# Kernel optimization log

Measured on AMD Instinct MI355X. Metric: run time of the kernel, lower is better.

Reference implementation:

```python
import jax, jax.numpy as jnp
import numpy as np

N_NODES = 100000
N_EDGES = 1600000
IN_DIM = 64
HEADS = [4, 4]
DIMS = [16, 16]


def gat_layer(x, src, dst, W, al, ar, b, n_nodes):
    """DGL-style GATConv: x [N,F] -> [N,H,D]."""
    H, D = al.shape
    z = (x @ W).reshape(-1, H, D)                      # [N,H,D]
    el = jnp.sum(z * al, axis=-1)                      # [N,H]
    er = jnp.sum(z * ar, axis=-1)                      # [N,H]
    e = jax.nn.leaky_relu(el[src] + er[dst], 0.2)      # [E,H] edge scores
    # numerically-stable edge softmax over incoming edges of each dst node
    m = jax.ops.segment_max(e, dst, num_segments=n_nodes)
    m = jnp.where(jnp.isfinite(m), m, 0.0)
    ex = jnp.exp(e - jax.lax.stop_gradient(m)[dst])    # [E,H]
    denom = jax.ops.segment_sum(ex, dst, num_segments=n_nodes)
    alpha = ex / jnp.maximum(denom[dst], 1e-9)         # [E,H]
    # scatter-aggregate messages alpha * z[src]
    out = jax.ops.segment_sum(alpha[:, :, None] * z[src], dst, num_segments=n_nodes)
    return out + b.reshape(H, D)


def setup_inputs() -> dict:
    key = jax.random.key(0)
    ks = jax.random.split(key, 16)
    feat = jax.random.normal(ks[0], (N_NODES, IN_DIM), dtype=jnp.float32)
    src = jax.random.randint(ks[1], (N_EDGES,), 0, N_NODES, dtype=jnp.int32)
    dst = jax.random.randint(ks[2], (N_EDGES,), 0, N_NODES, dtype=jnp.int32)
    def lin(k, fi, fo):
        return jax.random.normal(k, (fi, fo), dtype=jnp.float32) * (1.0 / np.sqrt(fi))
    H0, D0 = HEADS[0], DIMS[0]
    H1, D1 = HEADS[1], DIMS[1]
    inp = {
        "feat": feat, "src": src, "dst": dst,
        "W0": lin(ks[3], IN_DIM, H0 * D0),
        "al0": jax.random.normal(ks[4], (H0, D0), jnp.float32) * 0.1,
        "ar0": jax.random.normal(ks[5], (H0, D0), jnp.float32) * 0.1,
        "b0": jnp.zeros((H0 * D0,), jnp.float32),
        "W1": lin(ks[6], H0 * D0, H1 * D1),
        "al1": jax.random.normal(ks[7], (H1, D1), jnp.float32) * 0.1,
        "ar1": jax.random.normal(ks[8], (H1, D1), jnp.float32) * 0.1,
        "b1": jnp.zeros((H1 * D1,), jnp.float32),
        "Wo": lin(ks[9], H1 * D1, 1),
        "alo": jax.random.normal(ks[10], (1, 1), jnp.float32) * 0.1,
        "aro": jax.random.normal(ks[11], (1, 1), jnp.float32) * 0.1,
        "bo": jnp.zeros((1,), jnp.float32),
    }
    return inp


def reference(feat, src, dst, W0, al0, ar0, b0, W1, al1, ar1, b1, Wo, alo, aro, bo):
    n = feat.shape[0]
    h = gat_layer(feat, src, dst, W0, al0, ar0, b0, n)       # [N,H0,D0]
    h = jax.nn.relu(h).reshape(n, -1)                         # head concat
    h = gat_layer(h, src, dst, W1, al1, ar1, b1, n)           # [N,H1,D1]
    h = jax.nn.relu(h).reshape(n, -1)
    out = gat_layer(h, src, dst, Wo, alo, aro, bo, n)         # [N,1,1]
    return jnp.squeeze(out, axis=1)                           # [N,1]
```

## Files before the change

kernel.cpp:

```cpp
#include <hip/hip_runtime.h>
#include <hip/hip_fp16.h>
#include <math.h>

#define NN 100000
#define NE 1600000
#define NBUK 391
#define CAP 4608
#define EPB 4096

__device__ __forceinline__ float leaky02(float v) {
    return v > 0.0f ? v : 0.2f * v;
}


__global__ __launch_bounds__(256) void k_bucket(
    const int* __restrict__ src, const int* __restrict__ dst,
    int* __restrict__ bucketCnt, int* __restrict__ gBuf)
{
    __shared__ int stg[EPB];
    __shared__ int tgt[EPB];
    __shared__ int lcnt[NBUK];
    __shared__ int lexc[NBUK];
    __shared__ int lgb[NBUK];
    __shared__ int totalLocal;
    const int t = threadIdx.x;
    const int e0 = blockIdx.x * EPB;

    for (int i = t; i < NBUK; i += 256) lcnt[i] = 0;
    __syncthreads();

    int bk[16], pk[16];
    #pragma unroll
    for (int j = 0; j < 16; ++j) {
        const int e = e0 + j * 256 + t;
        if (e < NE) {
            const int d = dst[e];
            bk[j] = d >> 8;
            pk[j] = (src[e] << 8) | (d & 255);
            atomicAdd(&lcnt[bk[j]], 1);
        } else bk[j] = -1;
    }
    __syncthreads();

    if (t < 64) {
        int carry = 0;
        for (int c = 0; c < NBUK; c += 64) {
            const int idx = c + t;
            int v = (idx < NBUK) ? lcnt[idx] : 0;
            int inc = v;
            #pragma unroll
            for (int off = 1; off < 64; off <<= 1) {
                int u = __shfl_up(inc, off, 64);
                if (t >= off) inc += u;
            }
            if (idx < NBUK) lexc[idx] = carry + inc - v;
            carry += __shfl(inc, 63, 64);
        }
        if (t == 0) totalLocal = carry;
    }
    __syncthreads();

    for (int i = t; i < NBUK; i += 256) {
        const int c = lcnt[i];
        lgb[i] = c ? atomicAdd(&bucketCnt[i], c) : 0;
        lcnt[i] = 0;
    }
    __syncthreads();

    #pragma unroll
    for (int j = 0; j < 16; ++j) {
        if (bk[j] >= 0) {
            const int r = atomicAdd(&lcnt[bk[j]], 1);
            const int p = lexc[bk[j]] + r;
            stg[p] = pk[j];
            int slot = lgb[bk[j]] + r;
            if (slot >= CAP) slot = CAP - 1;
            tgt[p] = bk[j] * CAP + slot;
        }
    }
    __syncthreads();

    const int tot = totalLocal;
    for (int i = t; i < tot; i += 256)
        gBuf[tgt[i]] = stg[i];
}

__global__ __launch_bounds__(256) void k_csr_local(
    const int* __restrict__ bucketCnt, const int* __restrict__ gBuf,
    int* __restrict__ row_ptr, int* __restrict__ ssrc)
{
    __shared__ int stg2[CAP];
    __shared__ int stg3[CAP];
    __shared__ int c2[256];
    __shared__ int sc[256];
    __shared__ int red[256];
    const int t = threadIdx.x;
    const int k = blockIdx.x;
    const int cnt = min(bucketCnt[k], CAP);

    int part = 0;
    for (int j = t; j < k; j += 256) part += bucketCnt[j];
    red[t] = part;
    __syncthreads();
    for (int s2 = 128; s2; s2 >>= 1) {
        if (t < s2) red[t] += red[t + s2];
        __syncthreads();
    }
    const int gb = red[0];

    c2[t] = 0;
    __syncthreads();
    for (int i = t; i < cnt; i += 256) {
        const int pk = gBuf[k * CAP + i];
        stg2[i] = pk;
        atomicAdd(&c2[pk & 255], 1);
    }
    __syncthreads();
    if (t < 64) {
        int carry = 0;
        for (int c = 0; c < 256; c += 64) {
            int v = c2[c + t];
            int inc = v;
            #pragma unroll
            for (int off = 1; off < 64; off <<= 1) {
                int u = __shfl_up(inc, off, 64);
                if (t >= off) inc += u;
            }
            sc[c + t] = carry + inc - v;
            carry += __shfl(inc, 63, 64);
        }
    }
    __syncthreads();
    const int node = (k << 8) + t;
    if (node < NN) row_ptr[node] = gb + sc[t];
    if (k == NBUK - 1 && t == 0) row_ptr[NN] = NE;
    c2[t] = 0;
    __syncthreads();
    for (int i = t; i < cnt; i += 256) {
        const int pk = stg2[i];
        const int dl = pk & 255;
        const int r = atomicAdd(&c2[dl], 1);
        stg3[sc[dl] + r] = pk >> 8;
    }
    __syncthreads();
    for (int i = t; i < cnt; i += 256)
        ssrc[gb + i] = stg3[i];
}


__global__ __launch_bounds__(256) void k_node_prep(
    const float* __restrict__ xin, const float* __restrict__ W,
    const float* __restrict__ al, const float* __restrict__ ar,
    __half* __restrict__ z, float* __restrict__ el, float* __restrict__ er)
{
    const int t = threadIdx.x;
    const int lane = t & 63;
    const int wvU = __builtin_amdgcn_readfirstlane(t >> 6);
    const int nodeBase = blockIdx.x * 64 + wvU * 16;

    float wc[64];
    #pragma unroll
    for (int k = 0; k < 64; ++k) wc[k] = W[k * 64 + lane];
    const float a_l = al[lane], a_r = ar[lane];

    #pragma unroll 1
    for (int i = 0; i < 16; i += 2) {
        const int nA = nodeBase + i;
        if (nA >= NN) break;
        const int nB = nA + 1;
        const bool hasB = (nB < NN);
        const float4* __restrict__ xA4 = (const float4*)(xin + (size_t)nA * 64);
        const float4* __restrict__ xB4 = (const float4*)(xin + (size_t)(hasB ? nB : nA) * 64);

        float accA = 0.f, accB = 0.f;
        #pragma unroll
        for (int k4 = 0; k4 < 16; ++k4) {
            const float4 a4 = xA4[k4];
            const float4 b4 = xB4[k4];
            const float w0 = wc[k4 * 4 + 0], w1 = wc[k4 * 4 + 1];
            const float w2 = wc[k4 * 4 + 2], w3 = wc[k4 * 4 + 3];
            accA += a4.x * w0 + a4.y * w1 + a4.z * w2 + a4.w * w3;
            accB += b4.x * w0 + b4.y * w1 + b4.z * w2 + b4.w * w3;
        }

        {
            z[(size_t)nA * 64 + lane] = __float2half(accA);
            float pl = accA * a_l, pr = accA * a_r;
            #pragma unroll
            for (int off = 8; off > 0; off >>= 1) {
                pl += __shfl_xor(pl, off, 16);
                pr += __shfl_xor(pr, off, 16);
            }
            if ((lane & 15) == 0) {
                const int h = lane >> 4;
                el[nA * 4 + h] = pl;
                er[nA * 4 + h] = pr;
            }
        }
        if (hasB) {
            z[(size_t)nB * 64 + lane] = __float2half(accB);
            float pl = accB * a_l, pr = accB * a_r;
            #pragma unroll
            for (int off = 8; off > 0; off >>= 1) {
                pl += __shfl_xor(pl, off, 16);
                pr += __shfl_xor(pr, off, 16);
            }
            if ((lane & 15) == 0) {
                const int h = lane >> 4;
                el[nB * 4 + h] = pl;
                er[nB * 4 + h] = pr;
            }
        }
    }
}

__global__ __launch_bounds__(256) void k_csr_agg(
    const int* __restrict__ row_ptr, const int* __restrict__ ssrc,
    const float* __restrict__ el, const float* __restrict__ er,
    const __half* __restrict__ z, const float* __restrict__ b,
    float* __restrict__ xout,
    const float* __restrict__ Wo,
    float* __restrict__ zo)
{
    const int t = threadIdx.x;
    const int wv = t >> 6, l = t & 63;
    const int sg = l >> 4, sl = l & 15, hh = sl >> 2;
    const int n = blockIdx.x * 4 + wv;
    const int beg = row_ptr[n], end = row_ptr[n + 1];
    const float er_hh = er[n * 4 + hh];

    float4 acc = {0.f, 0.f, 0.f, 0.f};
    float den = 0.f;
    int i = beg + sg;
    for (; i + 12 < end; i += 16) {
        const int s0 = ssrc[i], s1 = ssrc[i + 4];
        const int s2 = ssrc[i + 8], s3 = ssrc[i + 12];
        const float x0 = __expf(leaky02(el[s0 * 4 + hh] + er_hh));
        const float x1 = __expf(leaky02(el[s1 * 4 + hh] + er_hh));
        const float x2 = __expf(leaky02(el[s2 * 4 + hh] + er_hh));
        const float x3 = __expf(leaky02(el[s3 * 4 + hh] + er_hh));
        const uint2 r0 = *(const uint2*)(z + (size_t)s0 * 64 + sl * 4);
        const uint2 r1 = *(const uint2*)(z + (size_t)s1 * 64 + sl * 4);
        const uint2 r2 = *(const uint2*)(z + (size_t)s2 * 64 + sl * 4);
        const uint2 r3 = *(const uint2*)(z + (size_t)s3 * 64 + sl * 4);
        den += (x0 + x1) + (x2 + x3);
        float2 p;
        p = __half22float2(*(const __half2*)&r0.x); acc.x += x0 * p.x; acc.y += x0 * p.y;
        p = __half22float2(*(const __half2*)&r0.y); acc.z += x0 * p.x; acc.w += x0 * p.y;
        p = __half22float2(*(const __half2*)&r1.x); acc.x += x1 * p.x; acc.y += x1 * p.y;
        p = __half22float2(*(const __half2*)&r1.y); acc.z += x1 * p.x; acc.w += x1 * p.y;
        p = __half22float2(*(const __half2*)&r2.x); acc.x += x2 * p.x; acc.y += x2 * p.y;
        p = __half22float2(*(const __half2*)&r2.y); acc.z += x2 * p.x; acc.w += x2 * p.y;
        p = __half22float2(*(const __half2*)&r3.x); acc.x += x3 * p.x; acc.y += x3 * p.y;
        p = __half22float2(*(const __half2*)&r3.y); acc.z += x3 * p.x; acc.w += x3 * p.y;
    }
    for (; i < end; i += 4) {
        const int s0 = ssrc[i];
        const float x0 = __expf(leaky02(el[s0 * 4 + hh] + er_hh));
        const uint2 r0 = *(const uint2*)(z + (size_t)s0 * 64 + sl * 4);
        den += x0;
        float2 p;
        p = __half22float2(*(const __half2*)&r0.x); acc.x += x0 * p.x; acc.y += x0 * p.y;
        p = __half22float2(*(const __half2*)&r0.y); acc.z += x0 * p.x; acc.w += x0 * p.y;
    }

    #pragma unroll
    for (int off = 16; off < 64; off <<= 1) {
        acc.x += __shfl_xor(acc.x, off, 64);
        acc.y += __shfl_xor(acc.y, off, 64);
        acc.z += __shfl_xor(acc.z, off, 64);
        acc.w += __shfl_xor(acc.w, off, 64);
        den   += __shfl_xor(den,   off, 64);
    }
    const float dinv = 1.0f / fmaxf(den, 1e-9f);

    const float4 b4 = *(const float4*)(b + sl * 4);
    float4 v;
    v.x = fmaxf(acc.x * dinv + b4.x, 0.f);
    v.y = fmaxf(acc.y * dinv + b4.y, 0.f);
    v.z = fmaxf(acc.z * dinv + b4.z, 0.f);
    v.w = fmaxf(acc.w * dinv + b4.w, 0.f);

    if (xout) {
        if (l < 16) *(float4*)(xout + (size_t)n * 64 + sl * 4) = v;
    } else {
        const float4 w4 = *(const float4*)(Wo + sl * 4);
        float p = v.x * w4.x + v.y * w4.y + v.z * w4.z + v.w * w4.w;
        #pragma unroll
        for (int off = 1; off < 16; off <<= 1) p += __shfl_xor(p, off, 64);
        if (l == 0) zo[n] = p;
    }
}


__global__ __launch_bounds__(256) void k_csr_agg_o(
    const int* __restrict__ row_ptr, const int* __restrict__ ssrc,
    const float* __restrict__ zo, const float* __restrict__ alo,
    const float* __restrict__ aro, const float* __restrict__ bo,
    float* __restrict__ out)
{
    const int t = threadIdx.x, l = t & 15;
    const int n = blockIdx.x * 16 + (t >> 4);
    const float a = alo[0];
    const float zr = aro[0] * zo[n];
    const int beg = row_ptr[n], end = row_ptr[n + 1];

    float den = 0.f, accv = 0.f;
    for (int i = beg + l; i < end; i += 16) {
        const float zs = zo[ssrc[i]];
        const float ex = __expf(leaky02(a * zs + zr));
        den += ex; accv += ex * zs;
    }
    #pragma unroll
    for (int off = 8; off; off >>= 1) {
        den  += __shfl_xor(den, off, 16);
        accv += __shfl_xor(accv, off, 16);
    }
    if (l == 0) out[n] = accv / fmaxf(den, 1e-9f) + bo[0];
}


extern "C" void kernel_launch(void* const* d_in, const int* in_sizes, int n_in,
                              void* d_out, int out_size, void* d_ws, size_t ws_size,
                              hipStream_t stream) {
    const float* feat = (const float*)d_in[0];
    const int*   src  = (const int*)d_in[1];
    const int*   dst  = (const int*)d_in[2];
    const float* W0   = (const float*)d_in[3];
    const float* al0  = (const float*)d_in[4];
    const float* ar0  = (const float*)d_in[5];
    const float* b0   = (const float*)d_in[6];
    const float* W1   = (const float*)d_in[7];
    const float* al1  = (const float*)d_in[8];
    const float* ar1  = (const float*)d_in[9];
    const float* b1   = (const float*)d_in[10];
    const float* Wo   = (const float*)d_in[11];
    const float* alo  = (const float*)d_in[12];
    const float* aro  = (const float*)d_in[13];
    const float* bo   = (const float*)d_in[14];
    float* out = (float*)d_out;

    int* bucketCnt  = (int*)d_ws;
    int* row_ptr    = bucketCnt + NBUK;
    int* gBuf       = row_ptr + (NN + 2);
    int* ssrc       = gBuf + (size_t)NBUK * CAP;
    uintptr_t pa = ((uintptr_t)(ssrc + NE) + 15) & ~(uintptr_t)15;
    __half* z  = (__half*)pa;
    float* xA  = (float*)(z + (size_t)NN * 64);
    float* el  = xA + (size_t)NN * 64;
    float* er  = el + (size_t)NN * 4;
    float* zo  = er + (size_t)NN * 4;

    const int gBkt  = (NE + EPB - 1) / EPB;
    const int gPrep = (NN + 63) / 64;
    const int gN16  = NN / 16;
    const int gAgg  = NN / 4;

    hipMemsetAsync(bucketCnt, 0, NBUK * sizeof(int), stream);
    k_bucket   <<<gBkt, 256, 0, stream>>>(src, dst, bucketCnt, gBuf);
    k_csr_local<<<NBUK, 256, 0, stream>>>(bucketCnt, gBuf, row_ptr, ssrc);

    k_node_prep<<<gPrep, 256, 0, stream>>>(feat, W0, al0, ar0, z, el, er);
    k_csr_agg  <<<gAgg, 256, 0, stream>>>(row_ptr, ssrc, el, er, z, b0,
                                          xA, nullptr, nullptr);

    k_node_prep<<<gPrep, 256, 0, stream>>>(xA, W1, al1, ar1, z, el, er);
    k_csr_agg  <<<gAgg, 256, 0, stream>>>(row_ptr, ssrc, el, er, z, b1,
                                          nullptr, Wo, zo);

    k_csr_agg_o<<<gN16, 256, 0, stream>>>(row_ptr, ssrc, zo, alo, aro, bo, out);
}
```

Before: 275.6 us.

## Fuse CSR build with layer-0 prep and split aggregation into two source-range passes

Bucketing and CSR construction now run in the same launches as the layer-0 node transform, so independent blocks overlap and two kernel boundaries disappear. The CSR also sorts each destination's edges by whether the source index falls in the lower or upper half of nodes. Aggregation then runs in two passes, one per source half, with partial sums stored in accT/denT. The aim is to shrink the gathered z working set per pass so it stays cache-resident, at the cost of extra launches and extra global traffic for the partial accumulators.

```diff
diff --git a/kernel.cpp b/kernel.cpp
--- a/kernel.cpp
+++ b/kernel.cpp
@@ -7,13 +7,17 @@
 #define NBUK 391
 #define CAP 4608
 #define EPB 4096
+#define FATA_PREP 782
+#define PREP_BLKS 1563
+#define SPLIT 50000
 
 __device__ __forceinline__ float leaky02(float v) {
     return v > 0.0f ? v : 0.2f * v;
 }
 
 
-__global__ __launch_bounds__(256) void k_bucket(
+__device__ __forceinline__ void bucket_body(
+    const int bid, const int t,
     const int* __restrict__ src, const int* __restrict__ dst,
     int* __restrict__ bucketCnt, int* __restrict__ gBuf)
 {
@@ -23,8 +27,7 @@
     __shared__ int lexc[NBUK];
     __shared__ int lgb[NBUK];
     __shared__ int totalLocal;
-    const int t = threadIdx.x;
-    const int e0 = blockIdx.x * EPB;
+    const int e0 = bid * EPB;
 
     for (int i = t; i < NBUK; i += 256) lcnt[i] = 0;
     __syncthreads();
@@ -85,17 +88,16 @@
         gBuf[tgt[i]] = stg[i];
 }
 
-__global__ __launch_bounds__(256) void k_csr_local(
+__device__ __forceinline__ void csr_body(
+    const int k, const int t,
     const int* __restrict__ bucketCnt, const int* __restrict__ gBuf,
-    int* __restrict__ row_ptr, int* __restrict__ ssrc)
+    int* __restrict__ row_ptr2, int* __restrict__ ssrc)
 {
     __shared__ int stg2[CAP];
     __shared__ int stg3[CAP];
-    __shared__ int c2[256];
-    __shared__ int sc[256];
+    __shared__ int c9[512];
+    __shared__ int sc9[512];
     __shared__ int red[256];
-    const int t = threadIdx.x;
-    const int k = blockIdx.x;
     const int cnt = min(bucketCnt[k], CAP);
 
     int part = 0;
@@ -108,55 +110,59 @@
     }
     const int gb = red[0];
 
-    c2[t] = 0;
+    c9[t] = 0; c9[t + 256] = 0;
     __syncthreads();
     for (int i = t; i < cnt; i += 256) {
         const int pk = gBuf[k * CAP + i];
         stg2[i] = pk;
-        atomicAdd(&c2[pk & 255], 1);
+        const int key = ((pk & 255) << 1) | ((pk >> 8) >= SPLIT ? 1 : 0);
+        atomicAdd(&c9[key], 1);
     }
     __syncthreads();
     if (t < 64) {
         int carry = 0;
-        for (int c = 0; c < 256; c += 64) {
-            int v = c2[c + t];
+        for (int c = 0; c < 512; c += 64) {
+            int v = c9[c + t];
             int inc = v;
             #pragma unroll
             for (int off = 1; off < 64; off <<= 1) {
                 int u = __shfl_up(inc, off, 64);
                 if (t >= off) inc += u;
             }
-            sc[c + t] = carry + inc - v;
+            sc9[c + t] = carry + inc - v;
             carry += __shfl(inc, 63, 64);
         }
     }
     __syncthreads();
-    const int node = (k << 8) + t;
-    if (node < NN) row_ptr[node] = gb + sc[t];
-    if (k == NBUK - 1 && t == 0) row_ptr[NN] = NE;
-    c2[t] = 0;
+    #pragma unroll
+    for (int j = 0; j < 2; ++j) {
+        const int i = t + 256 * j;
+        const int node = (k << 8) + (i >> 1);
+        if (node < NN) row_ptr2[node * 2 + (i & 1)] = gb + sc9[i];
+    }
+    if (k == NBUK - 1 && t == 0) row_ptr2[2 * NN] = NE;
+    c9[t] = 0; c9[t + 256] = 0;
     __syncthreads();
     for (int i = t; i < cnt; i += 256) {
         const int pk = stg2[i];
-        const int dl = pk & 255;
-        const int r = atomicAdd(&c2[dl], 1);
-        stg3[sc[dl] + r] = pk >> 8;
+        const int key = ((pk & 255) << 1) | ((pk >> 8) >= SPLIT ? 1 : 0);
+        const int r = atomicAdd(&c9[key], 1);
+        stg3[sc9[key] + r] = pk >> 8;
     }
     __syncthreads();
     for (int i = t; i < cnt; i += 256)
         ssrc[gb + i] = stg3[i];
 }
 
-
-__global__ __launch_bounds__(256) void k_node_prep(
+__device__ __forceinline__ void prep_body(
+    const int pb, const int t,
     const float* __restrict__ xin, const float* __restrict__ W,
     const float* __restrict__ al, const float* __restrict__ ar,
     __half* __restrict__ z, float* __restrict__ el, float* __restrict__ er)
 {
-    const int t = threadIdx.x;
     const int lane = t & 63;
     const int wvU = __builtin_amdgcn_readfirstlane(t >> 6);
-    const int nodeBase = blockIdx.x * 64 + wvU * 16;
+    const int nodeBase = pb * 64 + wvU * 16;
 
     float wc[64];
     #pragma unroll
@@ -214,10 +220,49 @@
     }
 }
 
-__global__ __launch_bounds__(256) void k_csr_agg(
-    const int* __restrict__ row_ptr, const int* __restrict__ ssrc,
+
+__global__ __launch_bounds__(256) void k_fatA(
+    const int* __restrict__ src, const int* __restrict__ dst,
+    int* __restrict__ bucketCnt, int* __restrict__ gBuf,
+    const float* __restrict__ feat, const float* __restrict__ W0,
+    const float* __restrict__ al0, const float* __restrict__ ar0,
+    __half* __restrict__ z, float* __restrict__ el, float* __restrict__ er)
+{
+    const int t = threadIdx.x;
+    if (blockIdx.x < NBUK)
+        bucket_body(blockIdx.x, t, src, dst, bucketCnt, gBuf);
+    else
+        prep_body(blockIdx.x - NBUK, t, feat, W0, al0, ar0, z, el, er);
+}
+
+__global__ __launch_bounds__(256) void k_fatB(
+    const int* __restrict__ bucketCnt, const int* __restrict__ gBuf,
+    int* __restrict__ row_ptr2, int* __restrict__ ssrc,
+    const float* __restrict__ feat, const float* __restrict__ W0,
+    const float* __restrict__ al0, const float* __restrict__ ar0,
+    __half* __restrict__ z, float* __restrict__ el, float* __restrict__ er)
+{
+    const int t = threadIdx.x;
+    if (blockIdx.x < NBUK)
+        csr_body(blockIdx.x, t, bucketCnt, gBuf, row_ptr2, ssrc);
+    else
+        prep_body(FATA_PREP + (blockIdx.x - NBUK), t, feat, W0, al0, ar0, z, el, er);
+}
+
+__global__ __launch_bounds__(256) void k_node_prep(
+    const float* __restrict__ xin, const float* __restrict__ W,
+    const float* __restrict__ al, const float* __restrict__ ar,
+    __half* __restrict__ z, float* __restrict__ el, float* __restrict__ er)
+{
+    prep_body(blockIdx.x, threadIdx.x, xin, W, al, ar, z, el, er);
+}
+
+__global__ __launch_bounds__(256) void k_agg_pass(
+    const int* __restrict__ row_ptr2, const int* __restrict__ ssrc,
     const float* __restrict__ el, const float* __restrict__ er,
     const __half* __restrict__ z, const float* __restrict__ b,
+    float* __restrict__ accT, float* __restrict__ denT,
+    const int pass,
     float* __restrict__ xout,
     const float* __restrict__ Wo,
     float* __restrict__ zo)
@@ -226,8 +271,16 @@
     const int wv = t >> 6, l = t & 63;
     const int sg = l >> 4, sl = l & 15, hh = sl >> 2;
     const int n = blockIdx.x * 4 + wv;
-    const int beg = row_ptr[n], end = row_ptr[n + 1];
+    const int beg = row_ptr2[2 * n + pass];
+    const int end = row_ptr2[2 * n + pass + 1];
     const float er_hh = er[n * 4 + hh];
+
+    float4 prev = {0.f, 0.f, 0.f, 0.f};
+    float denPrev = 0.f;
+    if (pass) {
+        prev = *(const float4*)(accT + (size_t)n * 64 + sl * 4);
+        denPrev = denT[n * 4 + hh];
+    }
 
     float4 acc = {0.f, 0.f, 0.f, 0.f};
     float den = 0.f;
@@ -272,6 +325,17 @@
         acc.w += __shfl_xor(acc.w, off, 64);
         den   += __shfl_xor(den,   off, 64);
     }
+
+    if (pass == 0) {
+        if (l < 16) {
+            *(float4*)(accT + (size_t)n * 64 + sl * 4) = acc;
+            if ((l & 3) == 0) denT[n * 4 + (l >> 2)] = den;
+        }
+        return;
+    }
+
+    acc.x += prev.x; acc.y += prev.y; acc.z += prev.z; acc.w += prev.w;
+    den += denPrev;
     const float dinv = 1.0f / fmaxf(den, 1e-9f);
 
     const float4 b4 = *(const float4*)(b + sl * 4);
@@ -294,7 +358,7 @@
 
 
 __global__ __launch_bounds__(256) void k_csr_agg_o(
-    const int* __restrict__ row_ptr, const int* __restrict__ ssrc,
+    const int* __restrict__ row_ptr2, const int* __restrict__ ssrc,
     const float* __restrict__ zo, const float* __restrict__ alo,
     const float* __restrict__ aro, const float* __restrict__ bo,
     float* __restrict__ out)
@@ -303,7 +367,7 @@
     const int n = blockIdx.x * 16 + (t >> 4);
     const float a = alo[0];
     const float zr = aro[0] * zo[n];
-    const int beg = row_ptr[n], end = row_ptr[n + 1];
+    const int beg = row_ptr2[2 * n], end = row_ptr2[2 * n + 2];
 
     float den = 0.f, accv = 0.f;
     for (int i = beg + l; i < end; i += 16) {
@@ -340,33 +404,41 @@
     const float* bo   = (const float*)d_in[14];
     float* out = (float*)d_out;
 
-    int* bucketCnt  = (int*)d_ws;
-    int* row_ptr    = bucketCnt + NBUK;
-    int* gBuf       = row_ptr + (NN + 2);
-    int* ssrc       = gBuf + (size_t)NBUK * CAP;
+    int* bucketCnt = (int*)d_ws;
+    int* row_ptr2  = bucketCnt + NBUK;
+    int* gBuf      = row_ptr2 + (2 * NN + 2);
+    int* ssrc      = gBuf + (size_t)NBUK * CAP;
     uintptr_t pa = ((uintptr_t)(ssrc + NE) + 15) & ~(uintptr_t)15;
     __half* z  = (__half*)pa;
     float* xA  = (float*)(z + (size_t)NN * 64);
     float* el  = xA + (size_t)NN * 64;
     float* er  = el + (size_t)NN * 4;
     float* zo  = er + (size_t)NN * 4;
-
-    const int gBkt  = (NE + EPB - 1) / EPB;
-    const int gPrep = (NN + 63) / 64;
+    float* accT = zo + NN;
+    float* denT = accT + (size_t)NN * 64;
+
+    const int gFatA = NBUK + FATA_PREP;
+    const int gFatB = NBUK + (PREP_BLKS - FATA_PREP);
     const int gN16  = NN / 16;
     const int gAgg  = NN / 4;
 
     hipMemsetAsync(bucketCnt, 0, NBUK * sizeof(int), stream);
-    k_bucket   <<<gBkt, 256, 0, stream>>>(src, dst, bucketCnt, gBuf);
-    k_csr_local<<<NBUK, 256, 0, stream>>>(bucketCnt, gBuf, row_ptr, ssrc);
-
-    k_node_prep<<<gPrep, 256, 0, stream>>>(feat, W0, al0, ar0, z, el, er);
-    k_csr_agg  <<<gAgg, 256, 0, stream>>>(row_ptr, ssrc, el, er, z, b0,
-                                          xA, nullptr, nullptr);
-
-    k_node_prep<<<gPrep, 256, 0, stream>>>(xA, W1, al1, ar1, z, el, er);
-    k_csr_agg  <<<gAgg, 256, 0, stream>>>(row_ptr, ssrc, el, er, z, b1,
-                                          nullptr, Wo, zo);
-
-    k_csr_agg_o<<<gN16, 256, 0, stream>>>(row_ptr, ssrc, zo, alo, aro, bo, out);
-}
+    k_fatA<<<gFatA, 256, 0, stream>>>(src, dst, bucketCnt, gBuf,
+                                      feat, W0, al0, ar0, z, el, er);
+    k_fatB<<<gFatB, 256, 0, stream>>>(bucketCnt, gBuf, row_ptr2, ssrc,
+                                      feat, W0, al0, ar0, z, el, er);
+
+    k_agg_pass<<<gAgg, 256, 0, stream>>>(row_ptr2, ssrc, el, er, z, b0,
+                                         accT, denT, 0, xA, nullptr, nullptr);
+    k_agg_pass<<<gAgg, 256, 0, stream>>>(row_ptr2, ssrc, el, er, z, b0,
+                                         accT, denT, 1, xA, nullptr, nullptr);
+
+    k_node_prep<<<PREP_BLKS, 256, 0, stream>>>(xA, W1, al1, ar1, z, el, er);
+
+    k_agg_pass<<<gAgg, 256, 0, stream>>>(row_ptr2, ssrc, el, er, z, b1,
+                                         accT, denT, 0, nullptr, Wo, zo);
+    k_agg_pass<<<gAgg, 256, 0, stream>>>(row_ptr2, ssrc, el, er, z, b1,
+                                         accT, denT, 1, nullptr, Wo, zo);
+
+    k_csr_agg_o<<<gN16, 256, 0, stream>>>(row_ptr2, ssrc, zo, alo, aro, bo, out);
+}
```

Result: slower. 327.7 us (+18.9%).
